# Kernel optimization log

Hardware: AMD Instinct MI355X
Metric: run time of the kernel (lower is better)

The kernel has to match this reference:

```python
import jax, jax.numpy as jnp
import numpy as np

EMB = 1024
HEADS = 16
HEAD_DIM = EMB // HEADS


def setup_inputs() -> dict:
    key = jax.random.key(0)
    ks = jax.random.split(key, 9)
    s = 1.0 / np.sqrt(EMB)
    x = jax.random.normal(ks[0], (2, 2048, EMB), dtype=jnp.float32)
    Wq = jax.random.normal(ks[1], (EMB, EMB), dtype=jnp.float32) * s
    bq = jnp.zeros((EMB,), dtype=jnp.float32)
    Wk = jax.random.normal(ks[2], (EMB, EMB), dtype=jnp.float32) * s
    bk = jnp.zeros((EMB,), dtype=jnp.float32)
    Wv = jax.random.normal(ks[3], (EMB, EMB), dtype=jnp.float32) * s
    bv = jnp.zeros((EMB,), dtype=jnp.float32)
    Wo = jax.random.normal(ks[4], (EMB, EMB), dtype=jnp.float32) * s
    bo = jnp.zeros((EMB,), dtype=jnp.float32)
    return {"x": x, "Wq": Wq, "bq": bq, "Wk": Wk, "bk": bk,
            "Wv": Wv, "bv": bv, "Wo": Wo, "bo": bo}


def reference(x, Wq, bq, Wk, bk, Wv, bv, Wo, bo):
    B, S, E = x.shape
    # torch Linear: y = x @ W.T + b
    q = x @ Wq.T + bq
    k = x @ Wk.T + bk
    v = x @ Wv.T + bv
    # [B,S,E] -> [B,H,S,D]
    q = q.reshape(B, S, HEADS, HEAD_DIM).transpose(0, 2, 1, 3)
    k = k.reshape(B, S, HEADS, HEAD_DIM).transpose(0, 2, 1, 3)
    v = v.reshape(B, S, HEADS, HEAD_DIM).transpose(0, 2, 1, 3)
    energy = jnp.einsum('bhqd,bhkd->bhqk', q, k)
    scaling = jnp.float32(E) ** 0.5  # NOTE: sqrt(emb_size), not sqrt(head_dim), as in source
    att = jax.nn.softmax(energy / scaling, axis=-1)
    out = jnp.einsum('bhqk,bhkd->bhqd', att, v)
    out = out.transpose(0, 2, 1, 3).reshape(B, S, E)
    return out @ Wo.T + bo
```

## Files before the change

kernel.cpp:

```cpp
#include <hip/hip_runtime.h>
#include <stdint.h>


typedef _Float16 half8  __attribute__((ext_vector_type(8)));
typedef _Float16 half4v __attribute__((ext_vector_type(4)));
typedef float    f32x4  __attribute__((ext_vector_type(4)));
typedef float    f32x16 __attribute__((ext_vector_type(16)));

#define GLD16(g, l) __builtin_amdgcn_global_load_lds(                         \
    (__attribute__((address_space(1))) void*)(g),                            \
    (__attribute__((address_space(3))) void*)(l), 16, 0, 0)

#define MFMA16(a, b, c) __builtin_amdgcn_mfma_f32_16x16x32_f16((a), (b), (c), 0, 0, 0)
#define MFMA32(a, b, c) __builtin_amdgcn_mfma_f32_32x32x16_f16((a), (b), (c), 0, 0, 0)

#if __has_builtin(__builtin_amdgcn_exp2f)
#define EXP2(x) __builtin_amdgcn_exp2f(x)
#else
#define EXP2(x) exp2f(x)
#endif

static __device__ inline uint32_t pk_u32(float a, float b)
{
    auto t = __builtin_amdgcn_cvt_pkrtz(a, b);
    return __builtin_bit_cast(uint32_t, t);
}

__global__ void cvt_all(const float* __restrict__ x,  const float* __restrict__ wq,
                        const float* __restrict__ wk, const float* __restrict__ wv,
                        const float* __restrict__ wo, _Float16* __restrict__ xb,
                        _Float16* __restrict__ wqkv, _Float16* __restrict__ wob)
{
    int i = blockIdx.x * blockDim.x + threadIdx.x;
    const float* src; _Float16* dst; int off;
    if (i < 1048576)      { src = x;  dst = xb;                 off = i; }
    else if (i < 1310720) { src = wq; dst = wqkv;               off = i - 1048576; }
    else if (i < 1572864) { src = wk; dst = wqkv + 1048576;     off = i - 1310720; }
    else if (i < 1835008) { src = wv; dst = wqkv + 2097152;     off = i - 1572864; }
    else                  { src = wo; dst = wob;                off = i - 1835008; }
    float4 f = ((const float4*)src)[off];
    half4v h = { (_Float16)f.x, (_Float16)f.y, (_Float16)f.z, (_Float16)f.w };
    ((half4v*)dst)[off] = h;
}

template<int BN, int MODE>
__global__ __launch_bounds__(256, MODE == 0 ? 3 : 2)
void gemm_f16(const _Float16* __restrict__ A, const _Float16* __restrict__ W,
              const float* __restrict__ b0, const float* __restrict__ b1,
              const float* __restrict__ b2, _Float16* __restrict__ o0,
              _Float16* __restrict__ o1, _Float16* __restrict__ o2,
              float* __restrict__ outf, float qscale)
{
    constexpr int NI = BN / 32;
    __shared__ _Float16 lA[128 * 64];
    __shared__ _Float16 lB[BN * 64];
    const int m0 = blockIdx.y * 128, n0 = blockIdx.x * BN;
    const int tid = threadIdx.x, lane = tid & 63, w = tid >> 6;
    const int wr = (w >> 1) * 64, wc = (w & 1) * (BN / 2);
    const int lrow = lane & 15, lk4 = lane >> 4;
    f32x4 acc[4][NI] = {};

    for (int k0 = 0; k0 < 1024; k0 += 64) {
        __syncthreads();
#pragma unroll
        for (int c = 0; c < 4; ++c) {
            int sidx = c * 256 + tid;
            int row = sidx >> 3, sl = sidx & 7;
            int gc = k0 + ((sl ^ (row & 7)) << 3);
            GLD16(A + (size_t)(m0 + row) * 1024 + gc, lA + (size_t)(c * 256 + w * 64) * 8);
        }
#pragma unroll
        for (int c = 0; c < BN / 32; ++c) {
            int sidx = c * 256 + tid;
            int row = sidx >> 3, sl = sidx & 7;
            int gc = k0 + ((sl ^ (row & 7)) << 3);
            GLD16(W + (size_t)(n0 + row) * 1024 + gc, lB + (size_t)(c * 256 + w * 64) * 8);
        }
        __syncthreads();

#pragma unroll
        for (int kd = 0; kd < 2; ++kd) {
            half8 af[4], bf[NI];
#pragma unroll
            for (int mi = 0; mi < 4; ++mi) {
                int ra = wr + mi * 16 + lrow;
                af[mi] = *(const half8*)(lA + ra * 64 + (((kd * 4 + lk4) ^ (ra & 7)) * 8));
            }
#pragma unroll
            for (int ni = 0; ni < NI; ++ni) {
                int rb = wc + ni * 16 + lrow;
                bf[ni] = *(const half8*)(lB + rb * 64 + (((kd * 4 + lk4) ^ (rb & 7)) * 8));
            }
#pragma unroll
            for (int mi = 0; mi < 4; ++mi)
#pragma unroll
                for (int ni = 0; ni < NI; ++ni)
                    acc[mi][ni] = MFMA16(af[mi], bf[ni], acc[mi][ni]);
        }
    }

    if (MODE == 0) {
        const int which = n0 >> 10;
        const float* bp = which == 0 ? b0 : which == 1 ? b1 : b2;
        const float scale = which == 0 ? qscale : 1.f;
        const int nh = n0 & 1023;
        float bcol[NI];
#pragma unroll
        for (int ni = 0; ni < NI; ++ni) bcol[ni] = bp[nh + wc + ni * 16 + lrow];
        if (which == 2) {
#pragma unroll
            for (int mi = 0; mi < 4; ++mi)
#pragma unroll
                for (int ni = 0; ni < NI; ++ni) {
                    int cg = nh + wc + ni * 16 + lrow;
                    int hh = cg >> 6, dd = cg & 63;
                    int sb = m0 + wr + mi * 16 + lk4 * 4;
                    int bb = sb >> 11, ss = sb & 2047;
                    int tile = ss >> 6, ks = (ss >> 4) & 3;
                    int hb = (ss >> 3) & 1, j0 = ss & 7;
                    int c2 = dd >> 5, l31v = dd & 31;
                    half4v pkv;
#pragma unroll
                    for (int r = 0; r < 4; ++r)
                        pkv[r] = (_Float16)(acc[mi][ni][r] + bcol[ni]);
                    size_t off = (size_t)(bb * 16 + hh) * 131072
                               + tile * 4096 + (ks * 2 + c2) * 512
                               + hb * 256 + l31v * 8 + j0;
                    *(half4v*)(o2 + off) = pkv;
                }
        } else if (which == 1) {
#pragma unroll
            for (int mi = 0; mi < 4; ++mi)
#pragma unroll
                for (int ni = 0; ni < NI; ++ni)
#pragma unroll
                    for (int r = 0; r < 4; ++r) {
                        int rg = m0 + wr + mi * 16 + lk4 * 4 + r;
                        int cg = nh + wc + ni * 16 + lrow;
                        float v = acc[mi][ni][r] + bcol[ni];
                        int bb = rg >> 11, ss = rg & 2047;
                        int hh = cg >> 6, dd = cg & 63;
                        int tile = ss >> 6, sbl = (ss >> 5) & 1, l31v = ss & 31;
                        int kd = dd >> 4, hv = (dd >> 3) & 1, jv = dd & 7;
                        size_t off = (size_t)(bb * 16 + hh) * 131072
                                   + tile * 4096 + (sbl * 4 + kd) * 512
                                   + hv * 256 + l31v * 8 + jv;
                        o1[off] = (_Float16)v;
                    }
        } else {
            _Float16* outh = o0;
#pragma unroll
            for (int mi = 0; mi < 4; ++mi)
#pragma unroll
                for (int ni = 0; ni < NI; ++ni)
#pragma unroll
                    for (int r = 0; r < 4; ++r) {
                        int rg = m0 + wr + mi * 16 + lk4 * 4 + r;
                        int cg = nh + wc + ni * 16 + lrow;
                        float v = (acc[mi][ni][r] + bcol[ni]) * scale;
                        int b = rg >> 11, s = rg & 2047, hh = cg >> 6, dd = cg & 63;
                        outh[(((size_t)b * 16 + hh) * 2048 + s) * 64 + dd] = (_Float16)v;
                    }
        }
    } else {
        float bcol[NI];
#pragma unroll
        for (int ni = 0; ni < NI; ++ni) bcol[ni] = b0[n0 + wc + ni * 16 + lrow];
#pragma unroll
        for (int mi = 0; mi < 4; ++mi)
#pragma unroll
            for (int ni = 0; ni < NI; ++ni)
#pragma unroll
                for (int r = 0; r < 4; ++r) {
                    int rg = m0 + wr + mi * 16 + lk4 * 4 + r;
                    int cg = n0 + wc + ni * 16 + lrow;
                    outf[(size_t)rg * 1024 + cg] = acc[mi][ni][r] + bcol[ni];
                }
    }
}

#define KVB 64
#define NT  32
__global__ __launch_bounds__(256, 4)
void attn(const _Float16* __restrict__ q, const _Float16* __restrict__ kf_,
          const _Float16* __restrict__ vf_, _Float16* __restrict__ ao)
{
    __shared__ _Float16 lKf[3 * 4096];
    const int bid0 = blockIdx.x;
    const int bid = (bid0 & 7) * 128 + (bid0 >> 3);
    const int bh = bid >> 5, q0 = (bid & 31) * 64;
    const int bb = bh >> 4, hh = bh & 15;
    const int tid = threadIdx.x, lane = tid & 63, w = tid >> 6;
    const int qb = w & 1, sh = w >> 1;
    const int l31 = lane & 31, h = lane >> 5;
    const _Float16* qh = q + (size_t)bh * 2048 * 64;
    const _Float16* khf = kf_ + (size_t)bh * 131072;
    const _Float16* vhf = vf_ + (size_t)bh * 131072;

    half8 qf[4];
#pragma unroll
    for (int kd = 0; kd < 4; ++kd)
        qf[kd] = *(const half8*)(qh + (size_t)(q0 + qb * 32 + l31) * 64
                                    + kd * 16 + h * 8);

    float l_ = 0.f;
    f32x16 o0 = {}, o1 = {};

    auto STAGEK = [&](int t, int bs) {
        const _Float16* src = khf + (size_t)t * 4096;
        _Float16* dst = lKf + bs * 4096;
#pragma unroll
        for (int c = 0; c < 2; ++c) {
            int p = c * 256 + tid;
            GLD16(src + (size_t)p * 8, dst + (size_t)p * 8);
        }
    };

    STAGEK(0, 0);
    STAGEK(1, 1);
    asm volatile("s_waitcnt vmcnt(2)" ::: "memory");

    for (int t = 0; t < NT; ++t) {
        const int cur = t % 3;
        __builtin_amdgcn_s_barrier();
        __builtin_amdgcn_sched_barrier(0);

        half8 vf[4];
        {
            const _Float16* src = vhf + (size_t)t * 4096 + (4 * sh) * 512 + lane * 8;
#pragma unroll
            for (int i = 0; i < 4; ++i)
                vf[i] = *(const half8*)(src + i * 512);
        }
        if (t + 2 < NT) STAGEK(t + 2, (t + 2) % 3);

        const _Float16* Kb = lKf + cur * 4096 + (sh * 4) * 512;
        half8 kf[4];
#pragma unroll
        for (int kd = 0; kd < 4; ++kd)
            kf[kd] = *(const half8*)(Kb + kd * 512 + lane * 8);

        f32x16 e = {};
        __builtin_amdgcn_s_setprio(1);
#pragma unroll
        for (int kd = 0; kd < 4; ++kd)
            e = MFMA32(kf[kd], qf[kd], e);
        __builtin_amdgcn_s_setprio(0);

        half8 pa[2];
        {
            float p[16];
#pragma unroll
            for (int r = 0; r < 16; ++r) p[r] = EXP2(e[r]);
            l_ += (((p[0] + p[1]) + (p[2] + p[3])) + ((p[4] + p[5]) + (p[6] + p[7])))
                + (((p[8] + p[9]) + (p[10] + p[11])) + ((p[12] + p[13]) + (p[14] + p[15])));
#pragma unroll
            for (int bq = 0; bq < 2; ++bq) {
                uint32_t w0 = pk_u32(p[bq * 8 + 0], p[bq * 8 + 1]);
                uint32_t w1 = pk_u32(p[bq * 8 + 2], p[bq * 8 + 3]);
                uint32_t w2 = pk_u32(p[bq * 8 + 4], p[bq * 8 + 5]);
                uint32_t w3 = pk_u32(p[bq * 8 + 6], p[bq * 8 + 7]);
                asm volatile("v_permlane32_swap_b32 %0, %1" : "+v"(w0), "+v"(w2));
                asm volatile("v_permlane32_swap_b32 %0, %1" : "+v"(w1), "+v"(w3));
                union { uint32_t u[4]; half8 hv; } uu;
                uu.u[0] = w0; uu.u[1] = w1; uu.u[2] = w2; uu.u[3] = w3;
                pa[bq] = uu.hv;
            }
        }

        if (t + 2 < NT) asm volatile("s_waitcnt vmcnt(2)" ::: "memory");
        else            asm volatile("s_waitcnt vmcnt(0)" ::: "memory");

        __builtin_amdgcn_s_setprio(1);
        o0 = MFMA32(pa[0], vf[0], o0);
        o1 = MFMA32(pa[0], vf[1], o1);
        o0 = MFMA32(pa[1], vf[2], o0);
        o1 = MFMA32(pa[1], vf[3], o1);
        __builtin_amdgcn_s_setprio(0);
    }

    l_ += __shfl_xor(l_, 32);
    __syncthreads();
    float* mO = (float*)lKf;
    float* mL = mO + 4096;
    if (sh == 1) {
#pragma unroll
        for (int r = 0; r < 16; ++r) {
            int qr = (r & 3) + 8 * (r >> 2) + 4 * h;
            mO[qb * 2048 + qr * 64 + l31]      = o0[r];
            mO[qb * 2048 + qr * 64 + 32 + l31] = o1[r];
        }
        if (h == 0) mL[qb * 32 + l31] = l_;
    }
    __syncthreads();
    if (sh == 0) {
        float ltot = l_ + mL[qb * 32 + l31];
        const size_t obase = ((size_t)bb * 2048) * 1024 + hh * 64;
#pragma unroll
        for (int r = 0; r < 16; ++r) {
            int qr = (r & 3) + 8 * (r >> 2) + 4 * h;
            float linv = 1.f / __shfl(ltot, qr);
            float v0 = o0[r] + mO[qb * 2048 + qr * 64 + l31];
            float v1 = o1[r] + mO[qb * 2048 + qr * 64 + 32 + l31];
            int sg = q0 + qb * 32 + qr;
            ao[obase + (size_t)sg * 1024 + l31]      = (_Float16)(v0 * linv);
            ao[obase + (size_t)sg * 1024 + 32 + l31] = (_Float16)(v1 * linv);
        }
    }
}

extern "C" void kernel_launch(void* const* d_in, const int* in_sizes, int n_in,
                              void* d_out, int out_size, void* d_ws, size_t ws_size,
                              hipStream_t stream)
{
    const float* x  = (const float*)d_in[0];
    const float* Wq = (const float*)d_in[1];
    const float* bq = (const float*)d_in[2];
    const float* Wk = (const float*)d_in[3];
    const float* bk = (const float*)d_in[4];
    const float* Wv = (const float*)d_in[5];
    const float* bv = (const float*)d_in[6];
    const float* Wo = (const float*)d_in[7];
    const float* bo = (const float*)d_in[8];
    float* out = (float*)d_out;

    char* ws = (char*)d_ws;
    _Float16* xb   = (_Float16*)(ws);
    _Float16* aob  = xb;
    _Float16* wqkv = (_Float16*)(ws + (8u  << 20));
    _Float16* wob  = (_Float16*)(ws + (14u << 20));
    _Float16* qb   = (_Float16*)(ws + (16u << 20));
    _Float16* kfb  = (_Float16*)(ws + (24u << 20));
    _Float16* vfb  = (_Float16*)(ws + (32u << 20));

    cvt_all<<<8192, 256, 0, stream>>>(x, Wq, Wk, Wv, Wo, xb, wqkv, wob);

    const float qscale = 1.4426950408889634f / 32.f;
    gemm_f16<128, 0><<<dim3(24, 32), 256, 0, stream>>>(
        xb, wqkv, bq, bk, bv, qb, kfb, vfb, nullptr, qscale);

    attn<<<1024, 256, 0, stream>>>(qb, kfb, vfb, aob);

    gemm_f16<64, 1><<<dim3(16, 32), 256, 0, stream>>>(
        aob, wob, bo, nullptr, nullptr, nullptr, nullptr, nullptr, out, 1.f);
}
```

Baseline: 112.4 us.

## Restructure attention with 128-query blocks, LDS-staged V, and software-pipelined QK/PV

Each attention block now handles 128 queries with four waves over the full KV tile, instead of splitting KV halves across waves. That removes the cross-wave LDS reduction at the end. V is now staged into LDS alongside K through a rotating triple buffer, and the loop is software-pipelined so the QK^T MFMAs for tile t+1 issue before the softmax and PV for tile t. The grid halves to 512 blocks and the occupancy hint drops to 2, trading parallelism and registers for better K/V reuse and overlap of exp work with matrix ops.

```diff
diff --git a/kernel.cpp b/kernel.cpp
--- a/kernel.cpp
+++ b/kernel.cpp
@@ -181,17 +181,16 @@
 
 #define KVB 64
 #define NT  32
-__global__ __launch_bounds__(256, 4)
+__global__ __launch_bounds__(256, 2)
 void attn(const _Float16* __restrict__ q, const _Float16* __restrict__ kf_,
           const _Float16* __restrict__ vf_, _Float16* __restrict__ ao)
 {
-    __shared__ _Float16 lKf[3 * 4096];
+    __shared__ _Float16 lKV[3 * 8192];
     const int bid0 = blockIdx.x;
-    const int bid = (bid0 & 7) * 128 + (bid0 >> 3);
-    const int bh = bid >> 5, q0 = (bid & 31) * 64;
+    const int bid = (bid0 & 7) * 64 + (bid0 >> 3);
+    const int bh = bid >> 4, q0 = (bid & 15) * 128;
     const int bb = bh >> 4, hh = bh & 15;
     const int tid = threadIdx.x, lane = tid & 63, w = tid >> 6;
-    const int qb = w & 1, sh = w >> 1;
     const int l31 = lane & 31, h = lane >> 5;
     const _Float16* qh = q + (size_t)bh * 2048 * 64;
     const _Float16* khf = kf_ + (size_t)bh * 131072;
@@ -200,58 +199,33 @@
     half8 qf[4];
 #pragma unroll
     for (int kd = 0; kd < 4; ++kd)
-        qf[kd] = *(const half8*)(qh + (size_t)(q0 + qb * 32 + l31) * 64
+        qf[kd] = *(const half8*)(qh + (size_t)(q0 + w * 32 + l31) * 64
                                     + kd * 16 + h * 8);
 
     float l_ = 0.f;
     f32x16 o0 = {}, o1 = {};
-
-    auto STAGEK = [&](int t, int bs) {
-        const _Float16* src = khf + (size_t)t * 4096;
-        _Float16* dst = lKf + bs * 4096;
+    f32x16 eA0 = {}, eA1 = {}, eB0 = {}, eB1 = {};
+
+    int sv = 0, sk = 1, sw = 2;
+
+    auto STAGE = [&](int t, int bs) {
+        const _Float16* ks = khf + (size_t)t * 4096;
+        const _Float16* vs = vhf + (size_t)t * 4096;
+        _Float16* dst = lKV + bs * 8192;
 #pragma unroll
         for (int c = 0; c < 2; ++c) {
             int p = c * 256 + tid;
-            GLD16(src + (size_t)p * 8, dst + (size_t)p * 8);
+            GLD16(ks + (size_t)p * 8, dst + (size_t)p * 8);
+            GLD16(vs + (size_t)p * 8, dst + 4096 + (size_t)p * 8);
         }
     };
 
-    STAGEK(0, 0);
-    STAGEK(1, 1);
-    asm volatile("s_waitcnt vmcnt(2)" ::: "memory");
-
-    for (int t = 0; t < NT; ++t) {
-        const int cur = t % 3;
-        __builtin_amdgcn_s_barrier();
-        __builtin_amdgcn_sched_barrier(0);
-
-        half8 vf[4];
-        {
-            const _Float16* src = vhf + (size_t)t * 4096 + (4 * sh) * 512 + lane * 8;
-#pragma unroll
-            for (int i = 0; i < 4; ++i)
-                vf[i] = *(const half8*)(src + i * 512);
-        }
-        if (t + 2 < NT) STAGEK(t + 2, (t + 2) % 3);
-
-        const _Float16* Kb = lKf + cur * 4096 + (sh * 4) * 512;
-        half8 kf[4];
-#pragma unroll
-        for (int kd = 0; kd < 4; ++kd)
-            kf[kd] = *(const half8*)(Kb + kd * 512 + lane * 8);
-
-        f32x16 e = {};
-        __builtin_amdgcn_s_setprio(1);
-#pragma unroll
-        for (int kd = 0; kd < 4; ++kd)
-            e = MFMA32(kf[kd], qf[kd], e);
-        __builtin_amdgcn_s_setprio(0);
-
-        half8 pa[2];
-        {
+    auto SOFTMAX = [&](const f32x16& ec0, const f32x16& ec1, half8 (&pa)[4]) {
+#pragma unroll
+        for (int f = 0; f < 2; ++f) {
             float p[16];
 #pragma unroll
-            for (int r = 0; r < 16; ++r) p[r] = EXP2(e[r]);
+            for (int r = 0; r < 16; ++r) p[r] = EXP2(f == 0 ? ec0[r] : ec1[r]);
             l_ += (((p[0] + p[1]) + (p[2] + p[3])) + ((p[4] + p[5]) + (p[6] + p[7])))
                 + (((p[8] + p[9]) + (p[10] + p[11])) + ((p[12] + p[13]) + (p[14] + p[15])));
 #pragma unroll
@@ -264,48 +238,103 @@
                 asm volatile("v_permlane32_swap_b32 %0, %1" : "+v"(w1), "+v"(w3));
                 union { uint32_t u[4]; half8 hv; } uu;
                 uu.u[0] = w0; uu.u[1] = w1; uu.u[2] = w2; uu.u[3] = w3;
-                pa[bq] = uu.hv;
+                pa[f * 2 + bq] = uu.hv;
             }
         }
-
-        if (t + 2 < NT) asm volatile("s_waitcnt vmcnt(2)" ::: "memory");
-        else            asm volatile("s_waitcnt vmcnt(0)" ::: "memory");
+    };
+
+    auto BODY = [&](int t, f32x16& ec0, f32x16& ec1, f32x16& en0, f32x16& en1)
+        __attribute__((always_inline))
+    {
+        asm volatile("s_waitcnt vmcnt(0)" ::: "memory");
+        __builtin_amdgcn_s_barrier();
+        __builtin_amdgcn_sched_barrier(0);
+        if (t + 2 < NT) STAGE(t + 2, sw);
+
+        const _Float16* Kb = lKV + sk * 8192;
+        const _Float16* Vb = lKV + sv * 8192 + 4096;
+        half8 kf[8], vf[8];
+#pragma unroll
+        for (int i = 0; i < 8; ++i)
+            kf[i] = *(const half8*)(Kb + i * 512 + lane * 8);
+#pragma unroll
+        for (int i = 0; i < 8; ++i)
+            vf[i] = *(const half8*)(Vb + i * 512 + lane * 8);
 
         __builtin_amdgcn_s_setprio(1);
-        o0 = MFMA32(pa[0], vf[0], o0);
-        o1 = MFMA32(pa[0], vf[1], o1);
-        o0 = MFMA32(pa[1], vf[2], o0);
-        o1 = MFMA32(pa[1], vf[3], o1);
+        en0 = MFMA32(kf[0], qf[0], f32x16{});
+        en1 = MFMA32(kf[4], qf[0], f32x16{});
+#pragma unroll
+        for (int kd = 1; kd < 4; ++kd) {
+            en0 = MFMA32(kf[kd], qf[kd], en0);
+            en1 = MFMA32(kf[4 + kd], qf[kd], en1);
+        }
         __builtin_amdgcn_s_setprio(0);
+
+        half8 pa[4];
+        SOFTMAX(ec0, ec1, pa);
+
+        __builtin_amdgcn_s_setprio(1);
+#pragma unroll
+        for (int ks = 0; ks < 4; ++ks) {
+            o0 = MFMA32(pa[ks], vf[ks * 2], o0);
+            o1 = MFMA32(pa[ks], vf[ks * 2 + 1], o1);
+        }
+        __builtin_amdgcn_s_setprio(0);
+
+        int tmp = sv; sv = sk; sk = sw; sw = tmp;
+    };
+
+    STAGE(0, 0);
+    STAGE(1, 1);
+    asm volatile("s_waitcnt vmcnt(0)" ::: "memory");
+    __builtin_amdgcn_s_barrier();
+    {
+        const _Float16* Kb = lKV;
+        half8 kf[8];
+#pragma unroll
+        for (int i = 0; i < 8; ++i)
+            kf[i] = *(const half8*)(Kb + i * 512 + lane * 8);
+        eA0 = MFMA32(kf[0], qf[0], f32x16{});
+        eA1 = MFMA32(kf[4], qf[0], f32x16{});
+#pragma unroll
+        for (int kd = 1; kd < 4; ++kd) {
+            eA0 = MFMA32(kf[kd], qf[kd], eA0);
+            eA1 = MFMA32(kf[4 + kd], qf[kd], eA1);
+        }
+    }
+
+#pragma unroll 1
+    for (int t = 0; t < 30; t += 2) {
+        BODY(t,     eA0, eA1, eB0, eB1);
+        BODY(t + 1, eB0, eB1, eA0, eA1);
+    }
+    BODY(30, eA0, eA1, eB0, eB1);
+
+    {
+        const _Float16* Vb = lKV + sv * 8192 + 4096;
+        half8 vf[8];
+#pragma unroll
+        for (int i = 0; i < 8; ++i)
+            vf[i] = *(const half8*)(Vb + i * 512 + lane * 8);
+        half8 pa[4];
+        SOFTMAX(eB0, eB1, pa);
+#pragma unroll
+        for (int ks = 0; ks < 4; ++ks) {
+            o0 = MFMA32(pa[ks], vf[ks * 2], o0);
+            o1 = MFMA32(pa[ks], vf[ks * 2 + 1], o1);
+        }
     }
 
     l_ += __shfl_xor(l_, 32);
-    __syncthreads();
-    float* mO = (float*)lKf;
-    float* mL = mO + 4096;
-    if (sh == 1) {
-#pragma unroll
-        for (int r = 0; r < 16; ++r) {
-            int qr = (r & 3) + 8 * (r >> 2) + 4 * h;
-            mO[qb * 2048 + qr * 64 + l31]      = o0[r];
-            mO[qb * 2048 + qr * 64 + 32 + l31] = o1[r];
-        }
-        if (h == 0) mL[qb * 32 + l31] = l_;
-    }
-    __syncthreads();
-    if (sh == 0) {
-        float ltot = l_ + mL[qb * 32 + l31];
-        const size_t obase = ((size_t)bb * 2048) * 1024 + hh * 64;
-#pragma unroll
-        for (int r = 0; r < 16; ++r) {
-            int qr = (r & 3) + 8 * (r >> 2) + 4 * h;
-            float linv = 1.f / __shfl(ltot, qr);
-            float v0 = o0[r] + mO[qb * 2048 + qr * 64 + l31];
-            float v1 = o1[r] + mO[qb * 2048 + qr * 64 + 32 + l31];
-            int sg = q0 + qb * 32 + qr;
-            ao[obase + (size_t)sg * 1024 + l31]      = (_Float16)(v0 * linv);
-            ao[obase + (size_t)sg * 1024 + 32 + l31] = (_Float16)(v1 * linv);
-        }
+    const size_t obase = ((size_t)bb * 2048) * 1024 + hh * 64;
+#pragma unroll
+    for (int r = 0; r < 16; ++r) {
+        int qr = (r & 3) + 8 * (r >> 2) + 4 * h;
+        float linv = 1.f / __shfl(l_, qr);
+        int sg = q0 + w * 32 + qr;
+        ao[obase + (size_t)sg * 1024 + l31]      = (_Float16)(o0[r] * linv);
+        ao[obase + (size_t)sg * 1024 + 32 + l31] = (_Float16)(o1[r] * linv);
     }
 }
 
@@ -339,7 +368,7 @@
     gemm_f16<128, 0><<<dim3(24, 32), 256, 0, stream>>>(
         xb, wqkv, bq, bk, bv, qb, kfb, vfb, nullptr, qscale);
 
-    attn<<<1024, 256, 0, stream>>>(qb, kfb, vfb, aob);
+    attn<<<512, 256, 0, stream>>>(qb, kfb, vfb, aob);
 
     gemm_f16<64, 1><<<dim3(16, 32), 256, 0, stream>>>(
         aob, wob, bo, nullptr, nullptr, nullptr, nullptr, nullptr, out, 1.f);
```

Measured after the change: 104.4 us. 7.1% less time.
